# Performance work log

Hardware: AMD Instinct MI355X
Metric: run time of the kernel (lower is better)

## Reference

```python
import jax, jax.numpy as jnp
import numpy as np

B, S, H, E = 4, 4096, 2048, 8
TOP_K = 2

def setup_inputs() -> dict:
    key = jax.random.key(0)
    k0, k1, k2, k3, k4 = jax.random.split(key, 5)
    Hm = H // 2
    return {
        "hidden_states": jax.random.normal(k0, (B, S, H), dtype=jnp.float32),
        "W1": jax.random.normal(k1, (H, Hm), dtype=jnp.float32) * (1.0 / np.sqrt(H)),
        "b1": jnp.zeros((Hm,), dtype=jnp.float32),
        "W2": jax.random.normal(k2, (Hm, E), dtype=jnp.float32) * (1.0 / np.sqrt(Hm)),
        "b2": jnp.zeros((E,), dtype=jnp.float32),
    }

def reference(hidden_states, W1, b1, W2, b2):
    # Router MLP: Linear(H -> H//2) -> ReLU -> Dropout(eval: identity) -> Linear(H//2 -> E)
    h = jax.nn.relu(jnp.einsum("bsh,hm->bsm", hidden_states, W1) + b1)
    router_logits = jnp.einsum("bsm,me->bse", h, W2) + b2  # [B, S, E]
    probs = jax.nn.softmax(router_logits, axis=-1)
    expert_weights, expert_indices = jax.lax.top_k(probs, TOP_K)  # [B, S, 2]
    return (router_logits, expert_weights, expert_indices)
```

## Files before the change

### kernel.cpp

```cpp
#include <hip/hip_runtime.h>
#include <hip/hip_bf16.h>


#define HDIM 2048
#define HM 1024
#define NROWS 16384
#define NE 8
#define KSTEPS 64

typedef _Float16 f16;
typedef f16 f16x8 __attribute__((ext_vector_type(8)));
typedef __fp16 h16x2 __attribute__((ext_vector_type(2)));
typedef float f32x4 __attribute__((ext_vector_type(4)));

union frag8 {
  f16x8 v;
  h16x2 p[4];
};

__device__ __forceinline__ void gload16(const void* g, void* l) {
  __builtin_amdgcn_global_load_lds(
      (const __attribute__((address_space(1))) void*)g,
      (__attribute__((address_space(3))) void*)l, 16, 0, 0);
}

__global__ __launch_bounds__(256) void prep_w1(const float* __restrict__ W1,
                                               f16* __restrict__ W1s) {
  const int nb = blockIdx.x & 3;
  const int ktidx = blockIdx.x >> 2;
  const int r = threadIdx.x;
  const int n = nb * 256 + r;
  const int kt = ktidx * 32;
  f16 hi[32], lo[32];
#pragma unroll
  for (int kk = 0; kk < 32; ++kk) {
    float x = W1[(size_t)(kt + kk) * HM + n];
    f16 h = (f16)x;
    hi[kk] = h;
    lo[kk] = (f16)(x - (float)h);
  }
  f16* dst = W1s + (size_t)(nb * 64 + ktidx) * 16384 + r * 64;
#pragma unroll
  for (int sp = 0; sp < 8; ++sp) {
    int s = sp ^ (r & 7);
    f16x8 v;
#pragma unroll
    for (int j = 0; j < 8; ++j)
      v[j] = (s < 4) ? hi[8 * s + j] : lo[8 * (s - 4) + j];
    *(f16x8*)(dst + sp * 8) = v;
  }
}

__global__ __launch_bounds__(512, 2) void router_mfma(
    const float* __restrict__ X, const f16* __restrict__ W1s,
    const float* __restrict__ b1, const float* __restrict__ W2,
    float* __restrict__ pl) {
  const int bid = blockIdx.x;
  const int wg = (bid & 7) * 32 + (bid >> 3);
  const int rb = wg >> 2;
  const int nb = wg & 3;

  const int t = threadIdx.x;
  const int lane = t & 63;
  const int wave = t >> 6;
  const int wm = wave >> 2;
  const int wn = wave & 3;
  const int lane15 = lane & 15;
  const int lgrp = lane >> 4;

  extern __shared__ char smem[];

  const int sa = (t & 7) ^ ((t >> 3) & 7);
  const float* Xp[4];
#pragma unroll
  for (int i = 0; i < 4; ++i)
    Xp[i] = X + (size_t)(rb * 256 + 64 * i + (t >> 3)) * HDIM + 4 * sa;
  const char* W1sB = (const char*)W1s + (size_t)nb * 64 * 32768;

  auto STAGE = [&](int buf, int ktidx) {
    char* bA = smem + buf * 65536;
    char* bB = bA + 32768;
    const int ktf = ktidx * 32;
#pragma unroll
    for (int i = 0; i < 4; ++i)
      gload16(Xp[i] + ktf, bA + i * 8192 + t * 16);
#pragma unroll
    for (int i = 0; i < 4; ++i)
      gload16(W1sB + ((size_t)ktidx << 15) + i * 8192 + t * 16,
              bB + i * 8192 + t * 16);
  };

  f32x4 acc[8][4];
#pragma unroll
  for (int i = 0; i < 8; ++i)
#pragma unroll
    for (int j = 0; j < 4; ++j) acc[i][j] = (f32x4){0.f, 0.f, 0.f, 0.f};

  STAGE(0, 0);
  STAGE(1, 1);
  asm volatile("s_waitcnt vmcnt(8)" ::: "memory");
  __builtin_amdgcn_s_barrier();

  int cur = 0;
  for (int kti = 0; kti < KSTEPS; ++kti) {
    const char* ldsA = smem + cur * 65536;
    const f16* ldsB = (const f16*)(ldsA + 32768);

    frag8 bh[4], bl[4];
#pragma unroll
    for (int ni = 0; ni < 4; ++ni) {
      int c = wn * 64 + ni * 16 + lane15;
      bh[ni].v = *(const f16x8*)&ldsB[c * 64 + ((lgrp ^ (c & 7)) << 3)];
      bl[ni].v = *(const f16x8*)&ldsB[c * 64 + (((4 + lgrp) ^ (c & 7)) << 3)];
    }

#pragma unroll
    for (int mi = 0; mi < 8; ++mi) {
      int r = wm * 128 + mi * 16 + lane15;
      const char* rowp = ldsA + r * 128;
      f32x4 va = *(const f32x4*)(rowp + ((((2 * lgrp) ^ (r & 7))) << 4));
      f32x4 vb = *(const f32x4*)(rowp + ((((2 * lgrp + 1) ^ (r & 7))) << 4));
      frag8 ah, al;
      h16x2 h0 = __builtin_amdgcn_cvt_pkrtz(va[0], va[1]);
      ah.p[0] = h0;
      al.p[0] = __builtin_amdgcn_cvt_pkrtz(va[0] - (float)h0[0],
                                           va[1] - (float)h0[1]);
      h16x2 h1 = __builtin_amdgcn_cvt_pkrtz(va[2], va[3]);
      ah.p[1] = h1;
      al.p[1] = __builtin_amdgcn_cvt_pkrtz(va[2] - (float)h1[0],
                                           va[3] - (float)h1[1]);
      h16x2 h2 = __builtin_amdgcn_cvt_pkrtz(vb[0], vb[1]);
      ah.p[2] = h2;
      al.p[2] = __builtin_amdgcn_cvt_pkrtz(vb[0] - (float)h2[0],
                                           vb[1] - (float)h2[1]);
      h16x2 h3 = __builtin_amdgcn_cvt_pkrtz(vb[2], vb[3]);
      ah.p[3] = h3;
      al.p[3] = __builtin_amdgcn_cvt_pkrtz(vb[2] - (float)h3[0],
                                           vb[3] - (float)h3[1]);
#pragma unroll
      for (int ni = 0; ni < 4; ++ni) {
        acc[mi][ni] = __builtin_amdgcn_mfma_f32_16x16x32_f16(
            ah.v, bh[ni].v, acc[mi][ni], 0, 0, 0);
        acc[mi][ni] = __builtin_amdgcn_mfma_f32_16x16x32_f16(
            ah.v, bl[ni].v, acc[mi][ni], 0, 0, 0);
        acc[mi][ni] = __builtin_amdgcn_mfma_f32_16x16x32_f16(
            al.v, bh[ni].v, acc[mi][ni], 0, 0, 0);
      }
    }

    if (kti == KSTEPS - 1) break;
    __builtin_amdgcn_sched_barrier(0);
    __builtin_amdgcn_s_barrier();
    if (kti + 2 < KSTEPS) {
      STAGE(cur, kti + 2);
      asm volatile("s_waitcnt vmcnt(8)" ::: "memory");
    } else {
      asm volatile("s_waitcnt vmcnt(0)" ::: "memory");
    }
    __builtin_amdgcn_s_barrier();
    cur ^= 1;
  }

  __syncthreads();
  float* red = (float*)smem;

  float bvals[4];
  float w2r[4][NE];
#pragma unroll
  for (int ni = 0; ni < 4; ++ni) {
    int c = nb * 256 + wn * 64 + ni * 16 + lane15;
    bvals[ni] = b1[c];
    const float* src = W2 + (size_t)c * NE;
#pragma unroll
    for (int e = 0; e < NE; ++e) w2r[ni][e] = src[e];
  }

#pragma unroll
  for (int mi = 0; mi < 8; ++mi) {
    float plr[4][NE];
#pragma unroll
    for (int j = 0; j < 4; ++j)
#pragma unroll
      for (int e = 0; e < NE; ++e) plr[j][e] = 0.f;
#pragma unroll
    for (int ni = 0; ni < 4; ++ni) {
#pragma unroll
      for (int j = 0; j < 4; ++j) {
        float h = acc[mi][ni][j] + bvals[ni];
        h = fmaxf(h, 0.f);
#pragma unroll
        for (int e = 0; e < NE; ++e) plr[j][e] = fmaf(h, w2r[ni][e], plr[j][e]);
      }
    }
#pragma unroll
    for (int m = 1; m < 16; m <<= 1)
#pragma unroll
      for (int j = 0; j < 4; ++j)
#pragma unroll
        for (int e = 0; e < NE; ++e)
          plr[j][e] += __shfl_xor(plr[j][e], m, 64);
    if (lane15 == 0) {
#pragma unroll
      for (int j = 0; j < 4; ++j) {
        int rr = wm * 128 + mi * 16 + lgrp * 4 + j;
#pragma unroll
        for (int e = 0; e < NE; ++e)
          red[(size_t)wn * 2048 + rr * NE + e] = plr[j][e];
      }
    }
  }
  __syncthreads();
  for (int i = t; i < 256 * NE; i += 512) {
    int r = i >> 3, e = i & 7;
    int row = rb * 256 + r;
    float s = red[i] + red[2048 + i] + red[4096 + i] + red[6144 + i];
    pl[((size_t)nb * NROWS + row) * NE + e] = s;
  }
}

__global__ __launch_bounds__(256) void router_finalize(
    const float* __restrict__ pl, const float* __restrict__ b2,
    float* __restrict__ out) {
  int row = blockIdx.x * 256 + threadIdx.x;
  if (row >= NROWS) return;
  float l[NE];
#pragma unroll
  for (int e = 0; e < NE; ++e) l[e] = b2[e];
  for (int nb = 0; nb < 4; ++nb) {
    const float* src = pl + ((size_t)nb * NROWS + row) * NE;
#pragma unroll
    for (int e = 0; e < NE; ++e) l[e] += src[e];
  }
#pragma unroll
  for (int e = 0; e < NE; ++e) out[(size_t)row * NE + e] = l[e];

  float m = l[0];
#pragma unroll
  for (int e = 1; e < NE; ++e) m = fmaxf(m, l[e]);
  float p[NE], s = 0.f;
#pragma unroll
  for (int e = 0; e < NE; ++e) {
    p[e] = expf(l[e] - m);
    s += p[e];
  }
  float inv = 1.f / s;

  float v0 = -1.f, v1 = -1.f;
  int i0 = 0, i1 = 0;
#pragma unroll
  for (int e = 0; e < NE; ++e) {
    float pe = p[e];
    if (pe > v0) {
      v1 = v0; i1 = i0;
      v0 = pe; i0 = e;
    } else if (pe > v1) {
      v1 = pe; i1 = e;
    }
  }
  size_t wbase = (size_t)NROWS * NE + (size_t)row * 2;
  out[wbase] = v0 * inv;
  out[wbase + 1] = v1 * inv;
  size_t ibase = (size_t)NROWS * NE + (size_t)NROWS * 2 + (size_t)row * 2;
  out[ibase] = (float)i0;
  out[ibase + 1] = (float)i1;
}

extern "C" void kernel_launch(void* const* d_in, const int* in_sizes, int n_in,
                              void* d_out, int out_size, void* d_ws,
                              size_t ws_size, hipStream_t stream) {
  const float* X = (const float*)d_in[0];
  const float* W1 = (const float*)d_in[1];
  const float* b1 = (const float*)d_in[2];
  const float* W2 = (const float*)d_in[3];
  const float* b2 = (const float*)d_in[4];
  float* out = (float*)d_out;

  float* pl = (float*)d_ws;
  f16* W1s = (f16*)((char*)d_ws + (size_t)4 * 1024 * 1024);

  (void)hipFuncSetAttribute((const void*)router_mfma,
                            hipFuncAttributeMaxDynamicSharedMemorySize, 131072);

  hipLaunchKernelGGL(prep_w1, dim3(256), dim3(256), 0, stream, W1, W1s);
  hipLaunchKernelGGL(router_mfma, dim3(256), dim3(512), 131072, stream, X, W1s,
                     b1, W2, pl);
  hipLaunchKernelGGL(router_finalize, dim3(NROWS / 256), dim3(256), 0, stream,
                     pl, b2, out);
}
```

Measured before the change: 213.5 us.

## Interleave next-tile global loads with MFMA phases and prefetch LDS A fragments

Restructures the K loop from a two-stage prefetch into a single-tile-ahead pipeline. Global-to-LDS loads for the next tile are spread across four MFMA phases, and A fragments for upcoming row groups are read from LDS while the current ones feed MFMAs, under explicit lgkmcnt waits and s_setprio. The goal is to hide LDS read latency and smooth memory issue, in exchange for less prefetch distance on global loads, more barriers per iteration and higher register pressure.

```diff
diff --git a/kernel.cpp b/kernel.cpp
--- a/kernel.cpp
+++ b/kernel.cpp
@@ -76,19 +76,7 @@
   for (int i = 0; i < 4; ++i)
     Xp[i] = X + (size_t)(rb * 256 + 64 * i + (t >> 3)) * HDIM + 4 * sa;
   const char* W1sB = (const char*)W1s + (size_t)nb * 64 * 32768;
-
-  auto STAGE = [&](int buf, int ktidx) {
-    char* bA = smem + buf * 65536;
-    char* bB = bA + 32768;
-    const int ktf = ktidx * 32;
-#pragma unroll
-    for (int i = 0; i < 4; ++i)
-      gload16(Xp[i] + ktf, bA + i * 8192 + t * 16);
-#pragma unroll
-    for (int i = 0; i < 4; ++i)
-      gload16(W1sB + ((size_t)ktidx << 15) + i * 8192 + t * 16,
-              bB + i * 8192 + t * 16);
-  };
+  const int t16 = t * 16;
 
   f32x4 acc[8][4];
 #pragma unroll
@@ -96,15 +84,74 @@
 #pragma unroll
     for (int j = 0; j < 4; ++j) acc[i][j] = (f32x4){0.f, 0.f, 0.f, 0.f};
 
-  STAGE(0, 0);
-  STAGE(1, 1);
-  asm volatile("s_waitcnt vmcnt(8)" ::: "memory");
+  const int arow_base = wm * 128 + lane15;
+  const int offA0 = ((2 * lgrp) ^ (lane15 & 7)) << 4;
+  const int offA1 = ((2 * lgrp + 1) ^ (lane15 & 7)) << 4;
+
+#define RDA(MI, VA, VB)                                                   \
+  {                                                                       \
+    const char* rp_ = ldsA + (arow_base + (MI) * 16) * 128;               \
+    VA = *(const f32x4*)(rp_ + offA0);                                    \
+    VB = *(const f32x4*)(rp_ + offA1);                                    \
+  }
+
+#define GL(G)                                                             \
+  {                                                                       \
+    if ((G) < 4)                                                          \
+      gload16(Xp[(G)] + (kti + 1) * 32, nb_base + (G) * 8192 + t16);      \
+    else                                                                  \
+      gload16(W1sB + (((size_t)(kti + 1)) << 15) + ((G) - 4) * 8192 +     \
+                  t16,                                                    \
+              nb_base + 32768 + ((G) - 4) * 8192 + t16);                  \
+  }
+
+#define SPLITMM(MI, VA, VB)                                               \
+  {                                                                       \
+    frag8 ah_, al_;                                                       \
+    h16x2 h0_ = __builtin_amdgcn_cvt_pkrtz(VA[0], VA[1]);                 \
+    ah_.p[0] = h0_;                                                       \
+    al_.p[0] = __builtin_amdgcn_cvt_pkrtz(VA[0] - (float)h0_[0],          \
+                                          VA[1] - (float)h0_[1]);         \
+    h16x2 h1_ = __builtin_amdgcn_cvt_pkrtz(VA[2], VA[3]);                 \
+    ah_.p[1] = h1_;                                                       \
+    al_.p[1] = __builtin_amdgcn_cvt_pkrtz(VA[2] - (float)h1_[0],          \
+                                          VA[3] - (float)h1_[1]);         \
+    h16x2 h2_ = __builtin_amdgcn_cvt_pkrtz(VB[0], VB[1]);                 \
+    ah_.p[2] = h2_;                                                       \
+    al_.p[2] = __builtin_amdgcn_cvt_pkrtz(VB[0] - (float)h2_[0],          \
+                                          VB[1] - (float)h2_[1]);         \
+    h16x2 h3_ = __builtin_amdgcn_cvt_pkrtz(VB[2], VB[3]);                 \
+    ah_.p[3] = h3_;                                                       \
+    al_.p[3] = __builtin_amdgcn_cvt_pkrtz(VB[2] - (float)h3_[0],          \
+                                          VB[3] - (float)h3_[1]);         \
+    _Pragma("unroll")                                                     \
+    for (int ni_ = 0; ni_ < 4; ++ni_) {                                   \
+      acc[(MI)][ni_] = __builtin_amdgcn_mfma_f32_16x16x32_f16(            \
+          ah_.v, bh[ni_].v, acc[(MI)][ni_], 0, 0, 0);                     \
+      acc[(MI)][ni_] = __builtin_amdgcn_mfma_f32_16x16x32_f16(            \
+          ah_.v, bl[ni_].v, acc[(MI)][ni_], 0, 0, 0);                     \
+      acc[(MI)][ni_] = __builtin_amdgcn_mfma_f32_16x16x32_f16(            \
+          al_.v, bh[ni_].v, acc[(MI)][ni_], 0, 0, 0);                     \
+    }                                                                     \
+  }
+
+#define LGKM(N) asm volatile("s_waitcnt lgkmcnt(" #N ")" ::: "memory")
+
+  {
+    char* nb_base = smem;
+    const int kti = -1;
+    GL(0); GL(1); GL(2); GL(3); GL(4); GL(5); GL(6); GL(7);
+  }
+  asm volatile("s_waitcnt vmcnt(0)" ::: "memory");
   __builtin_amdgcn_s_barrier();
 
   int cur = 0;
+#pragma unroll 1
   for (int kti = 0; kti < KSTEPS; ++kti) {
     const char* ldsA = smem + cur * 65536;
     const f16* ldsB = (const f16*)(ldsA + 32768);
+    char* nb_base = smem + (cur ^ 1) * 65536;
+    const bool hasNext = (kti + 1 < KSTEPS);
 
     frag8 bh[4], bl[4];
 #pragma unroll
@@ -113,51 +160,58 @@
       bh[ni].v = *(const f16x8*)&ldsB[c * 64 + ((lgrp ^ (c & 7)) << 3)];
       bl[ni].v = *(const f16x8*)&ldsB[c * 64 + (((4 + lgrp) ^ (c & 7)) << 3)];
     }
-
-#pragma unroll
-    for (int mi = 0; mi < 8; ++mi) {
-      int r = wm * 128 + mi * 16 + lane15;
-      const char* rowp = ldsA + r * 128;
-      f32x4 va = *(const f32x4*)(rowp + ((((2 * lgrp) ^ (r & 7))) << 4));
-      f32x4 vb = *(const f32x4*)(rowp + ((((2 * lgrp + 1) ^ (r & 7))) << 4));
-      frag8 ah, al;
-      h16x2 h0 = __builtin_amdgcn_cvt_pkrtz(va[0], va[1]);
-      ah.p[0] = h0;
-      al.p[0] = __builtin_amdgcn_cvt_pkrtz(va[0] - (float)h0[0],
-                                           va[1] - (float)h0[1]);
-      h16x2 h1 = __builtin_amdgcn_cvt_pkrtz(va[2], va[3]);
-      ah.p[1] = h1;
-      al.p[1] = __builtin_amdgcn_cvt_pkrtz(va[2] - (float)h1[0],
-                                           va[3] - (float)h1[1]);
-      h16x2 h2 = __builtin_amdgcn_cvt_pkrtz(vb[0], vb[1]);
-      ah.p[2] = h2;
-      al.p[2] = __builtin_amdgcn_cvt_pkrtz(vb[0] - (float)h2[0],
-                                           vb[1] - (float)h2[1]);
-      h16x2 h3 = __builtin_amdgcn_cvt_pkrtz(vb[2], vb[3]);
-      ah.p[3] = h3;
-      al.p[3] = __builtin_amdgcn_cvt_pkrtz(vb[2] - (float)h3[0],
-                                           vb[3] - (float)h3[1]);
-#pragma unroll
-      for (int ni = 0; ni < 4; ++ni) {
-        acc[mi][ni] = __builtin_amdgcn_mfma_f32_16x16x32_f16(
-            ah.v, bh[ni].v, acc[mi][ni], 0, 0, 0);
-        acc[mi][ni] = __builtin_amdgcn_mfma_f32_16x16x32_f16(
-            ah.v, bl[ni].v, acc[mi][ni], 0, 0, 0);
-        acc[mi][ni] = __builtin_amdgcn_mfma_f32_16x16x32_f16(
-            al.v, bh[ni].v, acc[mi][ni], 0, 0, 0);
-      }
-    }
-
-    if (kti == KSTEPS - 1) break;
+    f32x4 vA0, vB0, vA1, vB1, nA0, nB0, nA1, nB1;
+    RDA(0, vA0, vB0);
+    RDA(1, vA1, vB1);
+
+    RDA(2, nA0, nB0);
+    RDA(3, nA1, nB1);
+    if (hasNext) { GL(0); GL(1); GL(2); }
+    __builtin_amdgcn_s_barrier();
+    LGKM(4);
     __builtin_amdgcn_sched_barrier(0);
-    __builtin_amdgcn_s_barrier();
-    if (kti + 2 < KSTEPS) {
-      STAGE(cur, kti + 2);
-      asm volatile("s_waitcnt vmcnt(8)" ::: "memory");
-    } else {
-      asm volatile("s_waitcnt vmcnt(0)" ::: "memory");
-    }
-    __builtin_amdgcn_s_barrier();
+    __builtin_amdgcn_s_setprio(1);
+    SPLITMM(0, vA0, vB0);
+    SPLITMM(1, vA1, vB1);
+    __builtin_amdgcn_s_setprio(0);
+    __builtin_amdgcn_s_barrier();
+    vA0 = nA0; vB0 = nB0; vA1 = nA1; vB1 = nB1;
+
+    RDA(4, nA0, nB0);
+    RDA(5, nA1, nB1);
+    if (hasNext) { GL(3); GL(4); GL(5); }
+    __builtin_amdgcn_s_barrier();
+    LGKM(4);
+    __builtin_amdgcn_sched_barrier(0);
+    __builtin_amdgcn_s_setprio(1);
+    SPLITMM(2, vA0, vB0);
+    SPLITMM(3, vA1, vB1);
+    __builtin_amdgcn_s_setprio(0);
+    __builtin_amdgcn_s_barrier();
+    vA0 = nA0; vB0 = nB0; vA1 = nA1; vB1 = nB1;
+
+    RDA(6, nA0, nB0);
+    RDA(7, nA1, nB1);
+    if (hasNext) { GL(6); GL(7); }
+    __builtin_amdgcn_s_barrier();
+    LGKM(4);
+    __builtin_amdgcn_sched_barrier(0);
+    __builtin_amdgcn_s_setprio(1);
+    SPLITMM(4, vA0, vB0);
+    SPLITMM(5, vA1, vB1);
+    __builtin_amdgcn_s_setprio(0);
+    __builtin_amdgcn_s_barrier();
+    vA0 = nA0; vB0 = nB0; vA1 = nA1; vB1 = nB1;
+
+    LGKM(0);
+    __builtin_amdgcn_sched_barrier(0);
+    __builtin_amdgcn_s_setprio(1);
+    SPLITMM(6, vA0, vB0);
+    SPLITMM(7, vA1, vB1);
+    __builtin_amdgcn_s_setprio(0);
+    if (hasNext) asm volatile("s_waitcnt vmcnt(0)" ::: "memory");
+    __builtin_amdgcn_s_barrier();
+
     cur ^= 1;
   }
 
```

Measured after the change: 213.7 us. About the same (+0.1%).

## Pre-split X into fp16 hi/lo at staging time, register-prefetch A fragments

Applied to the files above, without the earlier changes.

X tiles are now loaded into registers two steps ahead, split once into fp16 hi/lo halves and written to LDS in swizzled f16 layout. This replaces the per-wave conversion of every A fragment inside the MFMA loop, which each of the four N-waves previously repeated. A fragments are double-buffered in registers across mi iterations, and MFMA sections are raised with s_setprio. The cost is higher register pressure from the in-flight X values and an extra LDS write phase with an lgkmcnt wait before the barrier.

```diff
diff --git a/kernel.cpp b/kernel.cpp
--- a/kernel.cpp
+++ b/kernel.cpp
@@ -70,25 +70,60 @@
 
   extern __shared__ char smem[];
 
-  const int sa = (t & 7) ^ ((t >> 3) & 7);
-  const float* Xp[4];
-#pragma unroll
-  for (int i = 0; i < 4; ++i)
-    Xp[i] = X + (size_t)(rb * 256 + 64 * i + (t >> 3)) * HDIM + 4 * sa;
+  const int srow = t >> 1;
+  const int shalf = t & 1;
+  const float* Xr = X + (size_t)(rb * 256 + srow) * HDIM + shalf * 16;
+  const int sm = srow & 7;
+  const int woff_h0 = srow * 128 + (((2 * shalf) ^ sm) << 4);
+  const int woff_h1 = srow * 128 + (((2 * shalf + 1) ^ sm) << 4);
+  const int woff_l0 = srow * 128 + (((4 + 2 * shalf) ^ sm) << 4);
+  const int woff_l1 = srow * 128 + (((5 + 2 * shalf) ^ sm) << 4);
+
   const char* W1sB = (const char*)W1s + (size_t)nb * 64 * 32768;
-
-  auto STAGE = [&](int buf, int ktidx) {
-    char* bA = smem + buf * 65536;
-    char* bB = bA + 32768;
-    const int ktf = ktidx * 32;
-#pragma unroll
-    for (int i = 0; i < 4; ++i)
-      gload16(Xp[i] + ktf, bA + i * 8192 + t * 16);
-#pragma unroll
-    for (int i = 0; i < 4; ++i)
-      gload16(W1sB + ((size_t)ktidx << 15) + i * 8192 + t * 16,
-              bB + i * 8192 + t * 16);
-  };
+  const int t16 = t * 16;
+
+#define GLB(KT, BUF)                                                      \
+  {                                                                       \
+    char* bB_ = smem + (BUF) * 65536 + 32768;                             \
+    _Pragma("unroll")                                                     \
+    for (int i_ = 0; i_ < 4; ++i_)                                        \
+      gload16(W1sB + (((size_t)(KT)) << 15) + i_ * 8192 + t16,            \
+              bB_ + i_ * 8192 + t16);                                     \
+  }
+
+#define SPLITWR(BUF, x0, x1, x2, x3)                                      \
+  {                                                                       \
+    char* bA_ = smem + (BUF) * 65536;                                     \
+    frag8 hi0_, hi1_, lo0_, lo1_;                                         \
+    hi0_.p[0] = __builtin_amdgcn_cvt_pkrtz(x0.x, x0.y);                   \
+    hi0_.p[1] = __builtin_amdgcn_cvt_pkrtz(x0.z, x0.w);                   \
+    hi0_.p[2] = __builtin_amdgcn_cvt_pkrtz(x1.x, x1.y);                   \
+    hi0_.p[3] = __builtin_amdgcn_cvt_pkrtz(x1.z, x1.w);                   \
+    hi1_.p[0] = __builtin_amdgcn_cvt_pkrtz(x2.x, x2.y);                   \
+    hi1_.p[1] = __builtin_amdgcn_cvt_pkrtz(x2.z, x2.w);                   \
+    hi1_.p[2] = __builtin_amdgcn_cvt_pkrtz(x3.x, x3.y);                   \
+    hi1_.p[3] = __builtin_amdgcn_cvt_pkrtz(x3.z, x3.w);                   \
+    lo0_.p[0] = __builtin_amdgcn_cvt_pkrtz(x0.x - (float)hi0_.p[0][0],    \
+                                           x0.y - (float)hi0_.p[0][1]);   \
+    lo0_.p[1] = __builtin_amdgcn_cvt_pkrtz(x0.z - (float)hi0_.p[1][0],    \
+                                           x0.w - (float)hi0_.p[1][1]);   \
+    lo0_.p[2] = __builtin_amdgcn_cvt_pkrtz(x1.x - (float)hi0_.p[2][0],    \
+                                           x1.y - (float)hi0_.p[2][1]);   \
+    lo0_.p[3] = __builtin_amdgcn_cvt_pkrtz(x1.z - (float)hi0_.p[3][0],    \
+                                           x1.w - (float)hi0_.p[3][1]);   \
+    lo1_.p[0] = __builtin_amdgcn_cvt_pkrtz(x2.x - (float)hi1_.p[0][0],    \
+                                           x2.y - (float)hi1_.p[0][1]);   \
+    lo1_.p[1] = __builtin_amdgcn_cvt_pkrtz(x2.z - (float)hi1_.p[1][0],    \
+                                           x2.w - (float)hi1_.p[1][1]);   \
+    lo1_.p[2] = __builtin_amdgcn_cvt_pkrtz(x3.x - (float)hi1_.p[2][0],    \
+                                           x3.y - (float)hi1_.p[2][1]);   \
+    lo1_.p[3] = __builtin_amdgcn_cvt_pkrtz(x3.z - (float)hi1_.p[3][0],    \
+                                           x3.w - (float)hi1_.p[3][1]);   \
+    *(f16x8*)(bA_ + woff_h0) = hi0_.v;                                    \
+    *(f16x8*)(bA_ + woff_h1) = hi1_.v;                                    \
+    *(f16x8*)(bA_ + woff_l0) = lo0_.v;                                    \
+    *(f16x8*)(bA_ + woff_l1) = lo1_.v;                                    \
+  }
 
   f32x4 acc[8][4];
 #pragma unroll
@@ -96,15 +131,43 @@
 #pragma unroll
     for (int j = 0; j < 4; ++j) acc[i][j] = (f32x4){0.f, 0.f, 0.f, 0.f};
 
-  STAGE(0, 0);
-  STAGE(1, 1);
-  asm volatile("s_waitcnt vmcnt(8)" ::: "memory");
+  {
+    GLB(0, 0);
+    GLB(1, 1);
+    float4 a0 = *(const float4*)(Xr + 0);
+    float4 a1 = *(const float4*)(Xr + 4);
+    float4 a2 = *(const float4*)(Xr + 8);
+    float4 a3 = *(const float4*)(Xr + 12);
+    float4 c0 = *(const float4*)(Xr + 32);
+    float4 c1 = *(const float4*)(Xr + 36);
+    float4 c2 = *(const float4*)(Xr + 40);
+    float4 c3 = *(const float4*)(Xr + 44);
+    asm volatile("s_waitcnt vmcnt(0)" ::: "memory");
+    SPLITWR(0, a0, a1, a2, a3);
+    SPLITWR(1, c0, c1, c2, c3);
+    asm volatile("s_waitcnt lgkmcnt(0)" ::: "memory");
+  }
   __builtin_amdgcn_s_barrier();
 
+  const int arow_base = wm * 128 + lane15;
+  const int offAh = ((lgrp ^ (lane15 & 7)) << 4);
+  const int offAl = (((4 + lgrp) ^ (lane15 & 7)) << 4);
+
   int cur = 0;
+#pragma unroll 1
   for (int kti = 0; kti < KSTEPS; ++kti) {
     const char* ldsA = smem + cur * 65536;
     const f16* ldsB = (const f16*)(ldsA + 32768);
+    const bool stage2 = (kti + 2 < KSTEPS);
+
+    float4 x0, x1, x2, x3;
+    if (stage2) {
+      const float* xs = Xr + (kti + 2) * 32;
+      x0 = *(const float4*)(xs + 0);
+      x1 = *(const float4*)(xs + 4);
+      x2 = *(const float4*)(xs + 8);
+      x3 = *(const float4*)(xs + 12);
+    }
 
     frag8 bh[4], bl[4];
 #pragma unroll
@@ -114,29 +177,20 @@
       bl[ni].v = *(const f16x8*)&ldsB[c * 64 + (((4 + lgrp) ^ (c & 7)) << 3)];
     }
 
+    frag8 ah, al, nah, nal;
+    {
+      const char* rowp = ldsA + arow_base * 128;
+      ah.v = *(const f16x8*)(rowp + offAh);
+      al.v = *(const f16x8*)(rowp + offAl);
+    }
 #pragma unroll
     for (int mi = 0; mi < 8; ++mi) {
-      int r = wm * 128 + mi * 16 + lane15;
-      const char* rowp = ldsA + r * 128;
-      f32x4 va = *(const f32x4*)(rowp + ((((2 * lgrp) ^ (r & 7))) << 4));
-      f32x4 vb = *(const f32x4*)(rowp + ((((2 * lgrp + 1) ^ (r & 7))) << 4));
-      frag8 ah, al;
-      h16x2 h0 = __builtin_amdgcn_cvt_pkrtz(va[0], va[1]);
-      ah.p[0] = h0;
-      al.p[0] = __builtin_amdgcn_cvt_pkrtz(va[0] - (float)h0[0],
-                                           va[1] - (float)h0[1]);
-      h16x2 h1 = __builtin_amdgcn_cvt_pkrtz(va[2], va[3]);
-      ah.p[1] = h1;
-      al.p[1] = __builtin_amdgcn_cvt_pkrtz(va[2] - (float)h1[0],
-                                           va[3] - (float)h1[1]);
-      h16x2 h2 = __builtin_amdgcn_cvt_pkrtz(vb[0], vb[1]);
-      ah.p[2] = h2;
-      al.p[2] = __builtin_amdgcn_cvt_pkrtz(vb[0] - (float)h2[0],
-                                           vb[1] - (float)h2[1]);
-      h16x2 h3 = __builtin_amdgcn_cvt_pkrtz(vb[2], vb[3]);
-      ah.p[3] = h3;
-      al.p[3] = __builtin_amdgcn_cvt_pkrtz(vb[2] - (float)h3[0],
-                                           vb[3] - (float)h3[1]);
+      if (mi < 7) {
+        const char* rowp = ldsA + (arow_base + (mi + 1) * 16) * 128;
+        nah.v = *(const f16x8*)(rowp + offAh);
+        nal.v = *(const f16x8*)(rowp + offAl);
+      }
+      __builtin_amdgcn_s_setprio(1);
 #pragma unroll
       for (int ni = 0; ni < 4; ++ni) {
         acc[mi][ni] = __builtin_amdgcn_mfma_f32_16x16x32_f16(
@@ -146,14 +200,19 @@
         acc[mi][ni] = __builtin_amdgcn_mfma_f32_16x16x32_f16(
             al.v, bh[ni].v, acc[mi][ni], 0, 0, 0);
       }
+      __builtin_amdgcn_s_setprio(0);
+      ah = nah;
+      al = nal;
     }
 
     if (kti == KSTEPS - 1) break;
     __builtin_amdgcn_sched_barrier(0);
     __builtin_amdgcn_s_barrier();
-    if (kti + 2 < KSTEPS) {
-      STAGE(cur, kti + 2);
-      asm volatile("s_waitcnt vmcnt(8)" ::: "memory");
+    if (stage2) {
+      GLB(kti + 2, cur);
+      asm volatile("s_waitcnt vmcnt(4)" ::: "memory");
+      SPLITWR(cur, x0, x1, x2, x3);
+      asm volatile("s_waitcnt lgkmcnt(0)" ::: "memory");
     } else {
       asm volatile("s_waitcnt vmcnt(0)" ::: "memory");
     }
```

Measured after the change: 206.1 us, median of 2. -3.5%, faster.
